# Kernel optimization log

Hardware: AMD Instinct MI355X
Metric: run time of the kernel (lower is better)

## Reference

```python
import jax, jax.numpy as jnp
import numpy as np

B, D, H = 8, 512, 8
HD = D // H            # 64 head dim
NS, NT = 8192, 4096    # search / template points
ATTN_EPS = 1e-6
LN_EPS = 1e-5


def layer_norm(x, g, b):
    m = jnp.mean(x, axis=-1, keepdims=True)
    v = jnp.mean((x - m) ** 2, axis=-1, keepdims=True)
    return (x - m) * jax.lax.rsqrt(v + LN_EPS) * g + b


def setup_inputs() -> dict:
    key = jax.random.key(0)
    ks = jax.random.split(key, 20)
    s = 0.02
    return {
        "search_feat": jax.random.normal(ks[0], (B, D, NS), jnp.float32),
        "search_xyz": jax.random.uniform(ks[1], (B, NS, 3), jnp.float32),
        "template_feat": jax.random.normal(ks[2], (B, D, NT), jnp.float32),
        "template_xyz": jax.random.uniform(ks[3], (B, NT, 3), jnp.float32),
        "pos_w1": jax.random.normal(ks[4], (3, D), jnp.float32) * s,
        "pos_b1": jnp.zeros((D,), jnp.float32),
        "pos_w2": jax.random.normal(ks[5], (D, D), jnp.float32) * s,
        "pos_b2": jnp.zeros((D,), jnp.float32),
        "wq": jax.random.normal(ks[6], (D, D), jnp.float32) * s,
        "wk": jax.random.normal(ks[7], (D, D), jnp.float32) * s,
        "wv": jax.random.normal(ks[8], (D, D), jnp.float32) * s,
        "w_merge": jax.random.normal(ks[9], (D, D), jnp.float32) * s,
        "mlp_w1": jax.random.normal(ks[10], (2 * D, 2 * D), jnp.float32) * s,
        "mlp_w2": jax.random.normal(ks[11], (2 * D, D), jnp.float32) * s,
        "ln1_g": jnp.ones((D,), jnp.float32),
        "ln1_b": jnp.zeros((D,), jnp.float32),
        "ln2_g": jnp.ones((D,), jnp.float32),
        "ln2_b": jnp.zeros((D,), jnp.float32),
    }


def reference(search_feat, search_xyz, template_feat, template_xyz,
              pos_w1, pos_b1, pos_w2, pos_b2, wq, wk, wv, w_merge,
              mlp_w1, mlp_w2, ln1_g, ln1_b, ln2_g, ln2_b):
    bs = search_feat.shape[0]
    sf = jnp.transpose(search_feat, (0, 2, 1))    # [B, Ns, D]
    tf = jnp.transpose(template_feat, (0, 2, 1))  # [B, Nt, D]

    # positional MLP on template coordinates
    pos = jax.nn.relu(template_xyz @ pos_w1 + pos_b1) @ pos_w2 + pos_b2
    tf_pos = tf + pos

    q = (sf @ wq).reshape(bs, NS, H, HD)
    k = (tf @ wk).reshape(bs, NT, H, HD)
    v = (tf_pos @ wv).reshape(bs, NT, H, HD)

    # LoFTR-style linear attention: phi(x) = elu(x) + 1
    Q = jax.nn.elu(q) + 1.0
    K = jax.nn.elu(k) + 1.0
    v_len = v.shape[1]
    v_n = v / v_len
    KV = jnp.einsum("bshd,bshv->bhdv", K, v_n)                 # [B,H,d,d]
    Z = 1.0 / (jnp.einsum("blhd,bhd->blh", Q, K.sum(axis=1)) + ATTN_EPS)
    msg = jnp.einsum("blhd,bhdv->blhv", Q, KV) * Z[..., None] * v_len

    msg = msg.reshape(bs, NS, H * HD) @ w_merge
    msg = layer_norm(msg, ln1_g, ln1_b)
    cat = jnp.concatenate([sf, msg], axis=2)                    # [B,Ns,2D]
    msg = jax.nn.relu(cat @ mlp_w1) @ mlp_w2
    msg = layer_norm(msg, ln2_g, ln2_b)
    return jnp.transpose(sf + msg, (0, 2, 1))                   # [B,D,Ns]
```

## Files before the change

### kernel.cpp

```cpp
#include <hip/hip_runtime.h>
#include <stdint.h>
#include <stddef.h>


using ushort_t = unsigned short;
using short8 = __attribute__((ext_vector_type(8))) short;
using f32x4  = __attribute__((ext_vector_type(4))) float;

#define DEVI __device__ __forceinline__

DEVI float b2f(unsigned short u) {
    unsigned v = ((unsigned)u) << 16;
    return __builtin_bit_cast(float, v);
}
DEVI unsigned short f2b(float x) {
    unsigned u = __builtin_bit_cast(unsigned, x);
    u += 0x7FFFu + ((u >> 16) & 1u);
    return (unsigned short)(u >> 16);
}
DEVI void gload16(const void* g, void* l) {
    __builtin_amdgcn_global_load_lds(
        (const __attribute__((address_space(1))) unsigned*)g,
        (__attribute__((address_space(3))) unsigned*)l, 16, 0, 0);
}

template <int EPI>
__global__ __launch_bounds__(256, 4)
void gemm128(const ushort_t* __restrict__ A0, const ushort_t* __restrict__ A1,
             const ushort_t* __restrict__ Wt, ushort_t* __restrict__ C,
             const float* __restrict__ bias, const ushort_t* __restrict__ addm,
             int N, int K, int K0, int lda0, int lda1, int nn)
{
    __shared__ ushort_t As[128 * 64];
    __shared__ ushort_t Bs[128 * 64];
    const int tid = threadIdx.x;
    const int cpx = gridDim.x >> 3;
    const int lid = (blockIdx.x & 7) * cpx + (blockIdx.x >> 3);
    const int m0 = (lid / nn) * 128;
    const int n0 = (lid % nn) * 128;
    const int w = tid >> 6, l = tid & 63;
    const int wm = (w >> 1) * 64, wn = (w & 1) * 64;
    const int lr = l & 15, lg = l >> 4;
    const int srow = tid >> 3;
    const int sck  = (tid & 7) ^ (srow & 7);
    const int nk = K / 64;

    f32x4 acc[4][4] = {};

    for (int t = 0; t < nk; ++t) {
        const int kb = t * 64;
        {
            const ushort_t* p; int ld;
            if (kb < K0) { p = A0 + (size_t)m0 * lda0 + kb; ld = lda0; }
            else         { p = A1 + (size_t)m0 * lda1 + (kb - K0); ld = lda1; }
            p += (size_t)srow * ld + sck * 8;
#pragma unroll
            for (int j = 0; j < 4; j++)
                gload16(p + (size_t)(j * 32) * ld, (void*)(&As[j * 2048] + tid * 8));
            const ushort_t* q = Wt + (size_t)(n0 + srow) * K + kb + sck * 8;
#pragma unroll
            for (int j = 0; j < 4; j++)
                gload16(q + (size_t)(j * 32) * K, (void*)(&Bs[j * 2048] + tid * 8));
        }
        asm volatile("s_waitcnt vmcnt(0)" ::: "memory");
        __builtin_amdgcn_s_barrier();
#pragma unroll
        for (int ks = 0; ks < 2; ks++) {
            short8 a[4], b[4];
#pragma unroll
            for (int mf = 0; mf < 4; mf++) {
                const int r = wm + mf * 16 + lr;
                a[mf] = *(const short8*)&As[r * 64 + ((ks * 4 + lg) ^ (r & 7)) * 8];
            }
#pragma unroll
            for (int nf = 0; nf < 4; nf++) {
                const int r = wn + nf * 16 + lr;
                b[nf] = *(const short8*)&Bs[r * 64 + ((ks * 4 + lg) ^ (r & 7)) * 8];
            }
            __builtin_amdgcn_s_setprio(1);
#pragma unroll
            for (int mf = 0; mf < 4; mf++)
#pragma unroll
                for (int nf = 0; nf < 4; nf++)
                    acc[mf][nf] = __builtin_amdgcn_mfma_f32_16x16x32_bf16(
                        a[mf], b[nf], acc[mf][nf], 0, 0, 0);
            __builtin_amdgcn_s_setprio(0);
        }
        __builtin_amdgcn_s_barrier();
    }

#pragma unroll
    for (int mf = 0; mf < 4; mf++) {
#pragma unroll
        for (int i = 0; i < 4; i++) {
            const int m = m0 + wm + mf * 16 + lg * 4 + i;
#pragma unroll
            for (int nf = 0; nf < 4; nf++) {
                const int n = n0 + wn + nf * 16 + lr;
                float x = acc[mf][nf][i];
                if constexpr (EPI == 1) { x = x > 0.f ? x + 1.f : __expf(x); }
                if constexpr (EPI == 2) { x += bias[n] + b2f(addm[(size_t)m * N + n]); }
                if constexpr (EPI == 3) { x = fmaxf(x, 0.f); }
                C[(size_t)m * N + n] = f2b(x);
            }
        }
    }
}

__global__ __launch_bounds__(256, 4)
void gemm_proj(const ushort_t* __restrict__ sfT, const ushort_t* __restrict__ tfT,
               const ushort_t* __restrict__ P1,
               const ushort_t* __restrict__ wqT, const ushort_t* __restrict__ wkT,
               const ushort_t* __restrict__ pw2T,
               ushort_t* __restrict__ Qp, ushort_t* __restrict__ Kp,
               ushort_t* __restrict__ tfpos, const float* __restrict__ pos_b2)
{
    __shared__ ushort_t As[128 * 64];
    __shared__ ushort_t Bs[128 * 64];
    const int tid = threadIdx.x;
    const int cpx = gridDim.x >> 3;
    const int lid = (blockIdx.x & 7) * cpx + (blockIdx.x >> 3);
    const ushort_t* A0; const ushort_t* Wt; ushort_t* C; int loc; bool doElu;
    if (lid < 2048)      { loc = lid;        A0 = sfT; Wt = wqT;  C = Qp;    doElu = true; }
    else if (lid < 3072) { loc = lid - 2048; A0 = tfT; Wt = wkT;  C = Kp;    doElu = true; }
    else                 { loc = lid - 3072; A0 = P1;  Wt = pw2T; C = tfpos; doElu = false; }
    const int m0 = (loc >> 2) * 128;
    const int n0 = (loc & 3) * 128;
    const int w = tid >> 6, l = tid & 63;
    const int wm = (w >> 1) * 64, wn = (w & 1) * 64;
    const int lr = l & 15, lg = l >> 4;
    const int srow = tid >> 3;
    const int sck  = (tid & 7) ^ (srow & 7);

    f32x4 acc[4][4] = {};

    for (int t = 0; t < 8; ++t) {
        const int kb = t * 64;
        {
            const ushort_t* p = A0 + (size_t)(m0 + srow) * 512 + kb + sck * 8;
#pragma unroll
            for (int j = 0; j < 4; j++)
                gload16(p + (size_t)(j * 32) * 512, (void*)(&As[j * 2048] + tid * 8));
            const ushort_t* q = Wt + (size_t)(n0 + srow) * 512 + kb + sck * 8;
#pragma unroll
            for (int j = 0; j < 4; j++)
                gload16(q + (size_t)(j * 32) * 512, (void*)(&Bs[j * 2048] + tid * 8));
        }
        asm volatile("s_waitcnt vmcnt(0)" ::: "memory");
        __builtin_amdgcn_s_barrier();
#pragma unroll
        for (int ks = 0; ks < 2; ks++) {
            short8 a[4], b[4];
#pragma unroll
            for (int mf = 0; mf < 4; mf++) {
                const int r = wm + mf * 16 + lr;
                a[mf] = *(const short8*)&As[r * 64 + ((ks * 4 + lg) ^ (r & 7)) * 8];
            }
#pragma unroll
            for (int nf = 0; nf < 4; nf++) {
                const int r = wn + nf * 16 + lr;
                b[nf] = *(const short8*)&Bs[r * 64 + ((ks * 4 + lg) ^ (r & 7)) * 8];
            }
            __builtin_amdgcn_s_setprio(1);
#pragma unroll
            for (int mf = 0; mf < 4; mf++)
#pragma unroll
                for (int nf = 0; nf < 4; nf++)
                    acc[mf][nf] = __builtin_amdgcn_mfma_f32_16x16x32_bf16(
                        a[mf], b[nf], acc[mf][nf], 0, 0, 0);
            __builtin_amdgcn_s_setprio(0);
        }
        __builtin_amdgcn_s_barrier();
    }

#pragma unroll
    for (int mf = 0; mf < 4; mf++) {
#pragma unroll
        for (int i = 0; i < 4; i++) {
            const int m = m0 + wm + mf * 16 + lg * 4 + i;
#pragma unroll
            for (int nf = 0; nf < 4; nf++) {
                const int n = n0 + wn + nf * 16 + lr;
                float x = acc[mf][nf][i];
                if (doElu) {
                    x = x > 0.f ? x + 1.f : __expf(x);
                } else {
                    x += pos_b2[n] + b2f(tfT[(size_t)m * 512 + n]);
                }
                C[(size_t)m * 512 + n] = f2b(x);
            }
        }
    }
}

__global__ __launch_bounds__(256)
void prep(const float* __restrict__ sfeat, const float* __restrict__ tfeat,
          const float* __restrict__ xyz, const float* __restrict__ pw1,
          const float* __restrict__ pb1,
          const float* wq, const float* wk, const float* wv, const float* wm,
          const float* pw2, const float* w1, const float* w2,
          ushort_t* sfT, ushort_t* tfT, ushort_t* P1,
          ushort_t* wqT, ushort_t* wkT, ushort_t* wvT, ushort_t* wmT,
          ushort_t* pw2T, ushort_t* w1T, ushort_t* w2T)
{
    const int bid = blockIdx.x;
    const int t = threadIdx.x;
    if (bid >= 12992) {
        const int m = (bid - 12992) * 4 + (t >> 6);
        const int n0 = (t & 63) * 8;
        const float x = xyz[m * 3 + 0], y = xyz[m * 3 + 1], z = xyz[m * 3 + 2];
        short8 o;
#pragma unroll
        for (int j = 0; j < 8; j++) {
            const int n = n0 + j;
            float v = x * pw1[n] + y * pw1[512 + n] + z * pw1[1024 + n] + pb1[n];
            o[j] = (short)f2b(fmaxf(v, 0.f));
        }
        *(short8*)&P1[(size_t)m * 512 + n0] = o;
        return;
    }
    __shared__ float tile[64][65];
    const float* src; ushort_t* dst; int R, Cc, c0, r0;
    if (bid < 8192) {
        const int b = bid >> 10, rem = bid & 1023;
        src = sfeat + (size_t)b * 512 * 8192; dst = sfT + (size_t)b * 512 * 8192;
        R = 512; Cc = 8192; c0 = (rem & 127) * 64; r0 = (rem >> 7) * 64;
    } else if (bid < 12288) {
        const int lcl = bid - 8192; const int b = lcl >> 9, rem = lcl & 511;
        src = tfeat + (size_t)b * 512 * 4096; dst = tfT + (size_t)b * 512 * 4096;
        R = 512; Cc = 4096; c0 = (rem & 63) * 64; r0 = (rem >> 6) * 64;
    } else {
        const int lcl = bid - 12288;
        if (lcl < 320) {
            const int wsel = lcl >> 6, local = lcl & 63;
            const float* srcs[5] = {wq, wk, wv, wm, pw2};
            ushort_t* dsts[5] = {wqT, wkT, wvT, wmT, pw2T};
            src = srcs[wsel]; dst = dsts[wsel];
            R = 512; Cc = 512; c0 = (local & 7) * 64; r0 = (local >> 3) * 64;
        } else if (lcl < 576) {
            const int local = lcl - 320;
            src = w1; dst = w1T; R = 1024; Cc = 1024;
            c0 = (local & 15) * 64; r0 = (local >> 4) * 64;
        } else {
            const int local = lcl - 576;
            src = w2; dst = w2T; R = 1024; Cc = 512;
            c0 = (local & 7) * 64; r0 = (local >> 3) * 64;
        }
    }
#pragma unroll
    for (int i = 0; i < 4; i++) {
        const int r = (t >> 4) + i * 16;
        const int c = (t & 15) * 4;
        const float4 v = *(const float4*)&src[(size_t)(r0 + r) * Cc + c0 + c];
        tile[r][c + 0] = v.x; tile[r][c + 1] = v.y;
        tile[r][c + 2] = v.z; tile[r][c + 3] = v.w;
    }
    __syncthreads();
#pragma unroll
    for (int i = 0; i < 2; i++) {
        const int c = (t >> 3) + i * 32;
        const int rs = (t & 7) * 8;
        short8 o;
#pragma unroll
        for (int j = 0; j < 8; j++) o[j] = (short)f2b(tile[rs + j][c]);
        *(short8*)&dst[(size_t)(c0 + c) * R + r0 + rs] = o;
    }
}

__global__ __launch_bounds__(256)
void kv_partial(const ushort_t* __restrict__ Kp, const ushort_t* __restrict__ V,
                float* __restrict__ KVp, float* __restrict__ Ksp)
{
    __shared__ ushort_t Ks[256 * 64];
    __shared__ ushort_t Vs[256 * 64];
    const int t = threadIdx.x;
    const int sp = blockIdx.x, h = blockIdx.y, b = blockIdx.z;
    const int d0 = t >> 2, e0 = (t & 3) * 16;
    const int srow = t >> 3, scol = (t & 7) * 8;
    float acc[16] = {};
    float ksum = 0.f;
    for (int c = 0; c < 2; c++) {
        if (c) __syncthreads();
        const size_t sbase = (size_t)b * 4096 + sp * 512 + c * 256;
#pragma unroll
        for (int i = 0; i < 8; i++) {
            const size_t go = (sbase + i * 32 + srow) * 512 + h * 64 + scol;
            gload16(Kp + go, (void*)(&Ks[i * 2048] + t * 8));
            gload16(V + go, (void*)(&Vs[i * 2048] + t * 8));
        }
        __syncthreads();
        for (int s = 0; s < 256; s++) {
            const float k = b2f(Ks[s * 64 + d0]);
            if ((t & 3) == 0) ksum += k;
            const short8 v0 = *(const short8*)&Vs[s * 64 + e0];
            const short8 v1 = *(const short8*)&Vs[s * 64 + e0 + 8];
#pragma unroll
            for (int j = 0; j < 8; j++) {
                acc[j]     += k * b2f((unsigned short)v0[j]);
                acc[8 + j] += k * b2f((unsigned short)v1[j]);
            }
        }
    }
    const int bh = b * 8 + h;
    float* kvo = KVp + (((size_t)sp * 64 + bh) * 64 + d0) * 64 + e0;
#pragma unroll
    for (int j = 0; j < 16; j++) kvo[j] = acc[j];
    if ((t & 3) == 0) Ksp[((size_t)sp * 64 + bh) * 64 + d0] = ksum;
}

__global__ __launch_bounds__(256)
void kv_finalize(const float* __restrict__ KVp, const float* __restrict__ Ksp,
                 ushort_t* __restrict__ KVt)
{
    const int bh = blockIdx.x, t = threadIdx.x;
    ushort_t* o = KVt + (size_t)bh * 5120;
#pragma unroll
    for (int i = 0; i < 16; i++) {
        const int idx = i * 256 + t;
        const int e = idx >> 6, d = idx & 63;
        float s = 0.f;
#pragma unroll
        for (int sp = 0; sp < 8; sp++)
            s += KVp[(((size_t)sp * 64 + bh) * 64 + d) * 64 + e];
        o[idx] = f2b(s);
    }
    if (t < 64) {
        float s = 0.f;
#pragma unroll
        for (int sp = 0; sp < 8; sp++) s += Ksp[((size_t)sp * 64 + bh) * 64 + t];
        o[4096 + t] = f2b(s);
    }
    for (int idx = 4160 + t; idx < 5120; idx += 256) o[idx] = 0;
}

__global__ __launch_bounds__(256, 2)
void attn_apply(const ushort_t* __restrict__ Qp, const ushort_t* __restrict__ KVt,
                ushort_t* __restrict__ msg1)
{
    __shared__ ushort_t As[256 * 64];
    __shared__ ushort_t Bs[80 * 64];
    const int t = threadIdx.x;
    const int ch = blockIdx.x, h = blockIdx.y, b = blockIdx.z;
    const int w = t >> 6, l = t & 63;
    const int lr = l & 15, lg = l >> 4;
    const int row0 = ch * 256;
    const int srow = t >> 3;
    const int sc = ((t & 7) ^ (srow & 7)) * 8;
    const ushort_t* kv = KVt + (size_t)(b * 8 + h) * 5120;
#pragma unroll
    for (int i = 0; i < 2; i++)
        gload16(kv + (size_t)(i * 32 + srow) * 64 + sc,
                (void*)(&Bs[i * 2048] + t * 8));
    if (t < 128)
        gload16(kv + (size_t)(64 + srow) * 64 + sc,
                (void*)(&Bs[4096] + t * 8));
    const ushort_t* qb = Qp + ((size_t)b * 8192 + row0) * 512 + h * 64;
#pragma unroll
    for (int i = 0; i < 8; i++)
        gload16(qb + (size_t)(i * 32 + srow) * 512 + sc,
                (void*)(&As[i * 2048] + t * 8));
    __syncthreads();
    f32x4 acc[4][5] = {};
    const int wr = w * 64;
#pragma unroll
    for (int ks = 0; ks < 2; ks++) {
        const int kswz = ((ks * 4 + lg) ^ (lr & 7)) * 8;
        short8 a[4], bb[5];
#pragma unroll
        for (int mf = 0; mf < 4; mf++)
            a[mf] = *(const short8*)&As[(wr + mf * 16 + lr) * 64 + kswz];
#pragma unroll
        for (int nf = 0; nf < 5; nf++)
            bb[nf] = *(const short8*)&Bs[(nf * 16 + lr) * 64 + kswz];
#pragma unroll
        for (int mf = 0; mf < 4; mf++)
#pragma unroll
            for (int nf = 0; nf < 5; nf++)
                acc[mf][nf] = __builtin_amdgcn_mfma_f32_16x16x32_bf16(
                    a[mf], bb[nf], acc[mf][nf], 0, 0, 0);
    }
#pragma unroll
    for (int mf = 0; mf < 4; mf++) {
#pragma unroll
        for (int i = 0; i < 4; i++) {
            const int m = row0 + wr + mf * 16 + lg * 4 + i;
            const float zden = __shfl(acc[mf][4][i], (l & 48));
            const float z = 1.f / (zden + 1e-6f);
#pragma unroll
            for (int nf = 0; nf < 4; nf++) {
                const int e = nf * 16 + lr;
                msg1[((size_t)b * 8192 + m) * 512 + h * 64 + e] =
                    f2b(acc[mf][nf][i] * z);
            }
        }
    }
}

__global__ __launch_bounds__(256)
void layer_norm_k(ushort_t* __restrict__ X, const float* __restrict__ g,
                  const float* __restrict__ bta)
{
    const int t = threadIdx.x;
    const int row = blockIdx.x * 4 + (t >> 6);
    const int l = t & 63;
    ushort_t* x = X + (size_t)row * 512;
    const short8 v = *(const short8*)&x[l * 8];
    float f[8];
    float s = 0.f;
#pragma unroll
    for (int j = 0; j < 8; j++) { f[j] = b2f((unsigned short)v[j]); s += f[j]; }
#pragma unroll
    for (int o = 32; o > 0; o >>= 1) s += __shfl_xor(s, o);
    const float mean = s * (1.f / 512.f);
    float vs = 0.f;
#pragma unroll
    for (int j = 0; j < 8; j++) { const float d = f[j] - mean; vs += d * d; }
#pragma unroll
    for (int o = 32; o > 0; o >>= 1) vs += __shfl_xor(vs, o);
    const float rstd = rsqrtf(vs * (1.f / 512.f) + 1e-5f);
    short8 ov;
#pragma unroll
    for (int j = 0; j < 8; j++) {
        const int c = l * 8 + j;
        ov[j] = (short)f2b((f[j] - mean) * rstd * g[c] + bta[c]);
    }
    *(short8*)&x[l * 8] = ov;
}

__global__ __launch_bounds__(256)
void ln2_final(const ushort_t* __restrict__ outp, const ushort_t* __restrict__ sfT,
               const float* __restrict__ g, const float* __restrict__ bta,
               float* __restrict__ out)
{
    __shared__ ushort_t tile[64][514];
    const int t = threadIdx.x;
    const int ns0 = blockIdx.x * 64, b = blockIdx.y;
    const int w = t >> 6, l = t & 63;
#pragma unroll
    for (int rr = 0; rr < 16; rr++) {
        const int r = w * 16 + rr;
        const size_t grow = (size_t)b * 8192 + ns0 + r;
        const short8 v = *(const short8*)&outp[grow * 512 + l * 8];
        float f[8];
        float s = 0.f;
#pragma unroll
        for (int j = 0; j < 8; j++) { f[j] = b2f((unsigned short)v[j]); s += f[j]; }
#pragma unroll
        for (int o = 32; o > 0; o >>= 1) s += __shfl_xor(s, o);
        const float mean = s * (1.f / 512.f);
        float vs = 0.f;
#pragma unroll
        for (int j = 0; j < 8; j++) { const float d = f[j] - mean; vs += d * d; }
#pragma unroll
        for (int o = 32; o > 0; o >>= 1) vs += __shfl_xor(vs, o);
        const float rstd = rsqrtf(vs * (1.f / 512.f) + 1e-5f);
        const short8 sv = *(const short8*)&sfT[grow * 512 + l * 8];
        short8 ov;
#pragma unroll
        for (int j = 0; j < 8; j++) {
            const int c = l * 8 + j;
            ov[j] = (short)f2b(b2f((unsigned short)sv[j]) +
                               (f[j] - mean) * rstd * g[c] + bta[c]);
        }
        *(short8*)&tile[r][l * 8] = ov;
    }
    __syncthreads();
#pragma unroll
    for (int i = 0; i < 32; i++) {
        const int d = (t >> 4) + i * 16;
        const int nss = (t & 15) * 4;
        float4 o;
        o.x = b2f(tile[nss + 0][d]);
        o.y = b2f(tile[nss + 1][d]);
        o.z = b2f(tile[nss + 2][d]);
        o.w = b2f(tile[nss + 3][d]);
        *(float4*)&out[((size_t)b * 512 + d) * 8192 + ns0 + nss] = o;
    }
}

extern "C" void kernel_launch(void* const* d_in, const int* in_sizes, int n_in,
                              void* d_out, int out_size, void* d_ws, size_t ws_size,
                              hipStream_t stream)
{
    (void)in_sizes; (void)n_in; (void)out_size; (void)ws_size;
    const float* search_feat   = (const float*)d_in[0];
    const float* template_feat = (const float*)d_in[2];
    const float* template_xyz  = (const float*)d_in[3];
    const float* pos_w1  = (const float*)d_in[4];
    const float* pos_b1  = (const float*)d_in[5];
    const float* pos_w2  = (const float*)d_in[6];
    const float* pos_b2  = (const float*)d_in[7];
    const float* wq      = (const float*)d_in[8];
    const float* wk      = (const float*)d_in[9];
    const float* wv      = (const float*)d_in[10];
    const float* w_merge = (const float*)d_in[11];
    const float* mlp_w1  = (const float*)d_in[12];
    const float* mlp_w2  = (const float*)d_in[13];
    const float* ln1_g   = (const float*)d_in[14];
    const float* ln1_b   = (const float*)d_in[15];
    const float* ln2_g   = (const float*)d_in[16];
    const float* ln2_b   = (const float*)d_in[17];
    float* out = (float*)d_out;

    char* ws = (char*)d_ws;
    ushort_t* sfT    = (ushort_t*)(ws + 0);
    ushort_t* Qp     = (ushort_t*)(ws + 67108864);
    ushort_t* tfT    = (ushort_t*)(ws + 134217728);
    ushort_t* Kp     = (ushort_t*)(ws + 167772160);
    ushort_t* msg2   = (ushort_t*)(ws + 134217728);
    ushort_t* P1     = (ushort_t*)(ws + 201326592);
    ushort_t* Vv     = (ushort_t*)(ws + 201326592);
    ushort_t* tfpos  = (ushort_t*)(ws + 234881024);
    ushort_t* msg1   = (ushort_t*)(ws + 268435456);
    ushort_t* hidden = (ushort_t*)(ws + 201326592);
    ushort_t* outp   = Qp;
    ushort_t* wqT  = (ushort_t*)(ws + 335544320);
    ushort_t* wkT  = (ushort_t*)(ws + 336068608);
    ushort_t* wvT  = (ushort_t*)(ws + 336592896);
    ushort_t* wmT  = (ushort_t*)(ws + 337117184);
    ushort_t* pw2T = (ushort_t*)(ws + 337641472);
    ushort_t* w1T  = (ushort_t*)(ws + 338165760);
    ushort_t* w2T  = (ushort_t*)(ws + 340262912);
    float*    KVp  = (float*)(ws + 268435456);
    float*    Ksp  = (float*)(ws + 276824064);
    ushort_t* KVt  = (ushort_t*)(ws + 345571328);

    prep<<<dim3(21184), 256, 0, stream>>>(
        search_feat, template_feat, template_xyz, pos_w1, pos_b1,
        wq, wk, wv, w_merge, pos_w2, mlp_w1, mlp_w2,
        sfT, tfT, P1, wqT, wkT, wvT, wmT, pw2T, w1T, w2T);
    gemm_proj<<<dim3(4096), 256, 0, stream>>>(sfT, tfT, P1, wqT, wkT, pw2T,
                                              Qp, Kp, tfpos, pos_b2);
    gemm128<0><<<dim3(1024), 256, 0, stream>>>(tfpos, nullptr, wvT, Vv,
                                               nullptr, nullptr, 512, 512, 512, 512, 0, 4);
    kv_partial<<<dim3(8, 8, 8), 256, 0, stream>>>(Kp, Vv, KVp, Ksp);
    kv_finalize<<<dim3(64), 256, 0, stream>>>(KVp, Ksp, KVt);
    attn_apply<<<dim3(32, 8, 8), 256, 0, stream>>>(Qp, KVt, msg1);
    gemm128<0><<<dim3(2048), 256, 0, stream>>>(msg1, nullptr, wmT, msg2,
                                               nullptr, nullptr, 512, 512, 512, 512, 0, 4);
    layer_norm_k<<<dim3(16384), 256, 0, stream>>>(msg2, ln1_g, ln1_b);
    gemm128<3><<<dim3(4096), 256, 0, stream>>>(sfT, msg2, w1T, hidden,
                                               nullptr, nullptr, 1024, 1024, 512, 512, 512, 8);
    gemm128<0><<<dim3(2048), 256, 0, stream>>>(hidden, nullptr, w2T, outp,
                                               nullptr, nullptr, 512, 1024, 1024, 1024, 0, 4);
    ln2_final<<<dim3(128, 8), 256, 0, stream>>>(outp, sfT, ln2_g, ln2_b, out);
}
```

Before: 658.5 us.

## Fold positional MLP second layer into value projection weights

Rewrites v = (tf + relu(xyz W1 + b1) W2 + b2) Wv as a single K=1024 GEMM over [tf | P1] against [Wv ; W2·Wv], plus a precomputed bias b2·Wv. This removes the 1024-block pos-MLP GEMM and the tfpos round trip through memory. It costs a small 512x512x512 weight-product GEMM inside gemm_proj, a serial bias reduction in prep, and a longer K loop in the V GEMM. The weight product is rounded to bf16, which changes numerics slightly.

```diff
diff --git a/kernel.cpp b/kernel.cpp
--- a/kernel.cpp
+++ b/kernel.cpp
@@ -4,6 +4,7 @@
 
 
 using ushort_t = unsigned short;
+using short4v = __attribute__((ext_vector_type(4))) short;
 using short8 = __attribute__((ext_vector_type(8))) short;
 using f32x4  = __attribute__((ext_vector_type(4))) float;
 
@@ -27,9 +28,10 @@
 template <int EPI>
 __global__ __launch_bounds__(256, 4)
 void gemm128(const ushort_t* __restrict__ A0, const ushort_t* __restrict__ A1,
-             const ushort_t* __restrict__ Wt, ushort_t* __restrict__ C,
-             const float* __restrict__ bias, const ushort_t* __restrict__ addm,
-             int N, int K, int K0, int lda0, int lda1, int nn)
+             const ushort_t* __restrict__ W0, const ushort_t* __restrict__ W1,
+             ushort_t* __restrict__ C, const float* __restrict__ bias,
+             int N, int K, int K0, int lda0, int lda1,
+             int K0w, int ldw0, int ldw1, int nn)
 {
     __shared__ ushort_t As[128 * 64];
     __shared__ ushort_t Bs[128 * 64];
@@ -57,10 +59,13 @@
 #pragma unroll
             for (int j = 0; j < 4; j++)
                 gload16(p + (size_t)(j * 32) * ld, (void*)(&As[j * 2048] + tid * 8));
-            const ushort_t* q = Wt + (size_t)(n0 + srow) * K + kb + sck * 8;
+            const ushort_t* q; int ldw;
+            if (kb < K0w) { q = W0 + (size_t)n0 * ldw0 + kb; ldw = ldw0; }
+            else          { q = W1 + (size_t)n0 * ldw1 + (kb - K0w); ldw = ldw1; }
+            q += (size_t)srow * ldw + sck * 8;
 #pragma unroll
             for (int j = 0; j < 4; j++)
-                gload16(q + (size_t)(j * 32) * K, (void*)(&Bs[j * 2048] + tid * 8));
+                gload16(q + (size_t)(j * 32) * ldw, (void*)(&Bs[j * 2048] + tid * 8));
         }
         asm volatile("s_waitcnt vmcnt(0)" ::: "memory");
         __builtin_amdgcn_s_barrier();
@@ -99,8 +104,8 @@
                 const int n = n0 + wn + nf * 16 + lr;
                 float x = acc[mf][nf][i];
                 if constexpr (EPI == 1) { x = x > 0.f ? x + 1.f : __expf(x); }
-                if constexpr (EPI == 2) { x += bias[n] + b2f(addm[(size_t)m * N + n]); }
                 if constexpr (EPI == 3) { x = fmaxf(x, 0.f); }
+                if constexpr (EPI == 4) { x += bias[n]; }
                 C[(size_t)m * N + n] = f2b(x);
             }
         }
@@ -109,11 +114,10 @@
 
 __global__ __launch_bounds__(256, 4)
 void gemm_proj(const ushort_t* __restrict__ sfT, const ushort_t* __restrict__ tfT,
-               const ushort_t* __restrict__ P1,
+               const ushort_t* __restrict__ wvT, const ushort_t* __restrict__ pw2C,
                const ushort_t* __restrict__ wqT, const ushort_t* __restrict__ wkT,
-               const ushort_t* __restrict__ pw2T,
                ushort_t* __restrict__ Qp, ushort_t* __restrict__ Kp,
-               ushort_t* __restrict__ tfpos, const float* __restrict__ pos_b2)
+               ushort_t* __restrict__ wv2T)
 {
     __shared__ ushort_t As[128 * 64];
     __shared__ ushort_t Bs[128 * 64];
@@ -121,9 +125,9 @@
     const int cpx = gridDim.x >> 3;
     const int lid = (blockIdx.x & 7) * cpx + (blockIdx.x >> 3);
     const ushort_t* A0; const ushort_t* Wt; ushort_t* C; int loc; bool doElu;
-    if (lid < 2048)      { loc = lid;        A0 = sfT; Wt = wqT;  C = Qp;    doElu = true; }
-    else if (lid < 3072) { loc = lid - 2048; A0 = tfT; Wt = wkT;  C = Kp;    doElu = true; }
-    else                 { loc = lid - 3072; A0 = P1;  Wt = pw2T; C = tfpos; doElu = false; }
+    if (lid < 2048)      { loc = lid;        A0 = sfT; Wt = wqT;  C = Qp;   doElu = true; }
+    else if (lid < 3072) { loc = lid - 2048; A0 = tfT; Wt = wkT;  C = Kp;   doElu = true; }
+    else                 { loc = lid - 3072; A0 = wvT; Wt = pw2C; C = wv2T; doElu = false; }
     const int m0 = (loc >> 2) * 128;
     const int n0 = (loc & 3) * 128;
     const int w = tid >> 6, l = tid & 63;
@@ -182,11 +186,7 @@
             for (int nf = 0; nf < 4; nf++) {
                 const int n = n0 + wn + nf * 16 + lr;
                 float x = acc[mf][nf][i];
-                if (doElu) {
-                    x = x > 0.f ? x + 1.f : __expf(x);
-                } else {
-                    x += pos_b2[n] + b2f(tfT[(size_t)m * 512 + n]);
-                }
+                if (doElu) x = x > 0.f ? x + 1.f : __expf(x);
                 C[(size_t)m * 512 + n] = f2b(x);
             }
         }
@@ -196,15 +196,22 @@
 __global__ __launch_bounds__(256)
 void prep(const float* __restrict__ sfeat, const float* __restrict__ tfeat,
           const float* __restrict__ xyz, const float* __restrict__ pw1,
-          const float* __restrict__ pb1,
-          const float* wq, const float* wk, const float* wv, const float* wm,
+          const float* __restrict__ pb1, const float* __restrict__ pb2,
+          const float* wq, const float* wk, const float* wvf, const float* wm,
           const float* pw2, const float* w1, const float* w2,
           ushort_t* sfT, ushort_t* tfT, ushort_t* P1,
           ushort_t* wqT, ushort_t* wkT, ushort_t* wvT, ushort_t* wmT,
-          ushort_t* pw2T, ushort_t* w1T, ushort_t* w2T)
+          ushort_t* pw2C, ushort_t* w1T, ushort_t* w2T, float* bv)
 {
     const int bid = blockIdx.x;
     const int t = threadIdx.x;
+    if (bid >= 21184) {
+        const int n = (bid - 21184) * 256 + t;
+        float a = 0.f;
+        for (int j = 0; j < 512; j++) a += pb2[j] * wvf[(size_t)j * 512 + n];
+        bv[n] = a;
+        return;
+    }
     if (bid >= 12992) {
         const int m = (bid - 12992) * 4 + (t >> 6);
         const int n0 = (t & 63) * 8;
@@ -217,6 +224,21 @@
             o[j] = (short)f2b(fmaxf(v, 0.f));
         }
         *(short8*)&P1[(size_t)m * 512 + n0] = o;
+        return;
+    }
+    if (bid >= 12544 && bid < 12608) {
+        const int local = bid - 12544;
+        const int r0 = (local >> 3) * 64, c0 = (local & 7) * 64;
+#pragma unroll
+        for (int i = 0; i < 4; i++) {
+            const int r = r0 + (t >> 4) + i * 16;
+            const int c = c0 + (t & 15) * 4;
+            const float4 v = *(const float4*)&pw2[(size_t)r * 512 + c];
+            short4v o;
+            o[0] = (short)f2b(v.x); o[1] = (short)f2b(v.y);
+            o[2] = (short)f2b(v.z); o[3] = (short)f2b(v.w);
+            *(short4v*)&pw2C[(size_t)r * 512 + c] = o;
+        }
         return;
     }
     __shared__ float tile[64][65];
@@ -229,23 +251,21 @@
         const int lcl = bid - 8192; const int b = lcl >> 9, rem = lcl & 511;
         src = tfeat + (size_t)b * 512 * 4096; dst = tfT + (size_t)b * 512 * 4096;
         R = 512; Cc = 4096; c0 = (rem & 63) * 64; r0 = (rem >> 6) * 64;
+    } else if (bid < 12544) {
+        const int lcl = bid - 12288;
+        const int wsel = lcl >> 6, local = lcl & 63;
+        const float* srcs[4] = {wq, wk, wvf, wm};
+        ushort_t* dsts[4] = {wqT, wkT, wvT, wmT};
+        src = srcs[wsel]; dst = dsts[wsel];
+        R = 512; Cc = 512; c0 = (local & 7) * 64; r0 = (local >> 3) * 64;
+    } else if (bid < 12864) {
+        const int local = bid - 12608;
+        src = w1; dst = w1T; R = 1024; Cc = 1024;
+        c0 = (local & 15) * 64; r0 = (local >> 4) * 64;
     } else {
-        const int lcl = bid - 12288;
-        if (lcl < 320) {
-            const int wsel = lcl >> 6, local = lcl & 63;
-            const float* srcs[5] = {wq, wk, wv, wm, pw2};
-            ushort_t* dsts[5] = {wqT, wkT, wvT, wmT, pw2T};
-            src = srcs[wsel]; dst = dsts[wsel];
-            R = 512; Cc = 512; c0 = (local & 7) * 64; r0 = (local >> 3) * 64;
-        } else if (lcl < 576) {
-            const int local = lcl - 320;
-            src = w1; dst = w1T; R = 1024; Cc = 1024;
-            c0 = (local & 15) * 64; r0 = (local >> 4) * 64;
-        } else {
-            const int local = lcl - 576;
-            src = w2; dst = w2T; R = 1024; Cc = 512;
-            c0 = (local & 7) * 64; r0 = (local >> 3) * 64;
-        }
+        const int local = bid - 12864;
+        src = w2; dst = w2T; R = 1024; Cc = 512;
+        c0 = (local & 7) * 64; r0 = (local >> 3) * 64;
     }
 #pragma unroll
     for (int i = 0; i < 4; i++) {
@@ -509,8 +529,7 @@
     ushort_t* Kp     = (ushort_t*)(ws + 167772160);
     ushort_t* msg2   = (ushort_t*)(ws + 134217728);
     ushort_t* P1     = (ushort_t*)(ws + 201326592);
-    ushort_t* Vv     = (ushort_t*)(ws + 201326592);
-    ushort_t* tfpos  = (ushort_t*)(ws + 234881024);
+    ushort_t* Vv     = (ushort_t*)(ws + 234881024);
     ushort_t* msg1   = (ushort_t*)(ws + 268435456);
     ushort_t* hidden = (ushort_t*)(ws + 201326592);
     ushort_t* outp   = Qp;
@@ -518,30 +537,36 @@
     ushort_t* wkT  = (ushort_t*)(ws + 336068608);
     ushort_t* wvT  = (ushort_t*)(ws + 336592896);
     ushort_t* wmT  = (ushort_t*)(ws + 337117184);
-    ushort_t* pw2T = (ushort_t*)(ws + 337641472);
+    ushort_t* wv2T = (ushort_t*)(ws + 337641472);
     ushort_t* w1T  = (ushort_t*)(ws + 338165760);
     ushort_t* w2T  = (ushort_t*)(ws + 340262912);
+    ushort_t* pw2C = (ushort_t*)(ws + 341311488);
+    float*    bv   = (float*)(ws + 342097920);
     float*    KVp  = (float*)(ws + 268435456);
     float*    Ksp  = (float*)(ws + 276824064);
     ushort_t* KVt  = (ushort_t*)(ws + 345571328);
 
-    prep<<<dim3(21184), 256, 0, stream>>>(
-        search_feat, template_feat, template_xyz, pos_w1, pos_b1,
+    prep<<<dim3(21186), 256, 0, stream>>>(
+        search_feat, template_feat, template_xyz, pos_w1, pos_b1, pos_b2,
         wq, wk, wv, w_merge, pos_w2, mlp_w1, mlp_w2,
-        sfT, tfT, P1, wqT, wkT, wvT, wmT, pw2T, w1T, w2T);
-    gemm_proj<<<dim3(4096), 256, 0, stream>>>(sfT, tfT, P1, wqT, wkT, pw2T,
-                                              Qp, Kp, tfpos, pos_b2);
-    gemm128<0><<<dim3(1024), 256, 0, stream>>>(tfpos, nullptr, wvT, Vv,
-                                               nullptr, nullptr, 512, 512, 512, 512, 0, 4);
+        sfT, tfT, P1, wqT, wkT, wvT, wmT, pw2C, w1T, w2T, bv);
+    gemm_proj<<<dim3(3088), 256, 0, stream>>>(sfT, tfT, wvT, pw2C, wqT, wkT,
+                                              Qp, Kp, wv2T);
+    gemm128<4><<<dim3(1024), 256, 0, stream>>>(tfT, P1, wvT, wv2T, Vv, bv,
+                                               512, 1024, 512, 512, 512,
+                                               512, 512, 512, 4);
     kv_partial<<<dim3(8, 8, 8), 256, 0, stream>>>(Kp, Vv, KVp, Ksp);
     kv_finalize<<<dim3(64), 256, 0, stream>>>(KVp, Ksp, KVt);
     attn_apply<<<dim3(32, 8, 8), 256, 0, stream>>>(Qp, KVt, msg1);
-    gemm128<0><<<dim3(2048), 256, 0, stream>>>(msg1, nullptr, wmT, msg2,
-                                               nullptr, nullptr, 512, 512, 512, 512, 0, 4);
+    gemm128<0><<<dim3(2048), 256, 0, stream>>>(msg1, nullptr, wmT, wmT, msg2,
+                                               nullptr, 512, 512, 512, 512, 0,
+                                               512, 512, 512, 4);
     layer_norm_k<<<dim3(16384), 256, 0, stream>>>(msg2, ln1_g, ln1_b);
-    gemm128<3><<<dim3(4096), 256, 0, stream>>>(sfT, msg2, w1T, hidden,
-                                               nullptr, nullptr, 1024, 1024, 512, 512, 512, 8);
-    gemm128<0><<<dim3(2048), 256, 0, stream>>>(hidden, nullptr, w2T, outp,
-                                               nullptr, nullptr, 512, 1024, 1024, 1024, 0, 4);
+    gemm128<3><<<dim3(4096), 256, 0, stream>>>(sfT, msg2, w1T, w1T, hidden,
+                                               nullptr, 1024, 1024, 512, 512, 512,
+                                               1024, 1024, 1024, 8);
+    gemm128<0><<<dim3(2048), 256, 0, stream>>>(hidden, nullptr, w2T, w2T, outp,
+                                               nullptr, 512, 1024, 1024, 1024, 1024,
+                                               1024, 1024, 1024, 4);
     ln2_final<<<dim3(128, 8), 256, 0, stream>>>(outp, sfT, ln2_g, ln2_b, out);
 }
```

After: 648.0 us. No clear change (-1.6%).
